# Performance work log

Measured on AMD Instinct MI355X. Metric: run time of the kernel, lower is better.

## Reference

```python
import jax, jax.numpy as jnp
import numpy as np

# Central-difference gradients on a 5D field (b, d1, d2, d3, c); slices crop
# the two non-differentiated spatial axes by 1 on each side so all outputs align.

def grad_dx(f):
    return (f[:, 2:, 1:-1, 1:-1] - f[:, :-2, 1:-1, 1:-1]) * 0.5

def grad_dy(f):
    return (f[:, 1:-1, 2:, 1:-1] - f[:, 1:-1, :-2, 1:-1]) * 0.5

def grad_dz(f):
    return (f[:, 1:-1, 1:-1, 2:] - f[:, 1:-1, 1:-1, :-2]) * 0.5


def setup_inputs() -> dict:
    key = jax.random.key(0)
    ddf = jax.random.normal(key, (4, 160, 160, 160, 3), dtype=jnp.float32)
    return {"ddf": ddf}


def reference(ddf) -> jnp.ndarray:
    # first derivatives: (b, d-2, h-2, w-2, 3)
    dfdx = grad_dx(ddf)
    dfdy = grad_dy(ddf)
    dfdz = grad_dz(ddf)
    # second derivatives: (b, d-4, h-4, w-4, 3)
    dfdxx = grad_dx(dfdx)
    dfdyy = grad_dy(dfdy)
    dfdzz = grad_dz(dfdz)
    dfdxy = grad_dy(dfdx)
    dfdyz = grad_dz(dfdy)
    dfdxz = grad_dz(dfdx)
    energy = (dfdxx ** 2 + dfdyy ** 2 + dfdzz ** 2
              + 2.0 * dfdxy ** 2 + 2.0 * dfdxz ** 2 + 2.0 * dfdyz ** 2)
    return jnp.mean(energy, axis=(1, 2, 3, 4))  # shape (batch,)
```

## Files before the change

kernel.cpp:

```cpp
#include <hip/hip_runtime.h>


typedef float F4 __attribute__((ext_vector_type(4)));

#define DIM 160
#define SX (DIM * DIM * 3)
#define SY (DIM * 3)
#define FSZ ((long long)DIM * SX)
#define TOT (4LL * FSZ)

#define ROWS 20
#define ROWU 37
#define USED_U (ROWS * ROWU)
#define SLICE_U 744
#define SLICE_F (SLICE_U * 4)
#define SLOTS 6
#define STEPS 26
#define NSEG 6
#define NMS 4
#define NYT 10
#define NBLK (4 * NSEG * NMS * NYT)
#define CPX (NBLK / 8)

__global__ __launch_bounds__(256, 2) void be_kernel(const float* __restrict__ f,
                                                    float* __restrict__ out) {
    __shared__ float lds[SLICE_F * SLOTS];
    const int tid = threadIdx.x;

    int lid = (blockIdx.x & 7) * CPX + (blockIdx.x >> 3);
    int p2 = lid / (NMS * NYT);
    int q2 = lid % (NMS * NYT);
    int b = p2 / NSEG, xseg = p2 % NSEG;
    int ms = q2 / NYT, yt = q2 % NYT;

    const int X0 = 2 + xseg * STEPS;
    const int gy0 = 16 * yt;
    const int core = 4 + 128 * ms;
    const int Gm = core - 8;
    const long long bb = (long long)b * FSZ;
    const float* fend = f + (TOT - 4);

    const int t = tid >> 4;
    const int yy = tid & 15;
    const int m0 = core + 8 * t;
    const int y = 2 + 16 * yt + yy;

    int jlo = 6 - m0; if (jlo < 0) jlo = 0;
    int jhi = 474 - m0; if (jhi > 8) jhi = 8;
    if (y >= DIM - 2) jhi = -1;

    const int rc = (yy + 2) * ROWU + 2 * t;

    auto stage = [&](int slab) {
        int slot = slab % SLOTS;
        long long gbase = bb + (long long)slab * SX + Gm;
#pragma unroll
        for (int it = 0; it < 3; ++it) {
            int c = it * 256 + tid;
            if (c < USED_U) {
                int row = c / ROWU;
                int col = c - row * ROWU;
                const float* gp = f + (gbase + (long long)(gy0 + row) * SY + 4 * col);
                gp = gp < f ? f : gp;
                gp = gp > fend ? fend : gp;
                __builtin_amdgcn_global_load_lds(
                    (const __attribute__((address_space(1))) unsigned int*)gp,
                    (__attribute__((address_space(3))) unsigned int*)
                        ((__attribute__((address_space(3))) float*)lds
                         + slot * SLICE_F + 4 * c),
                    16, 0, 0);
            }
        }
    };

    for (int d = -2; d <= 2; ++d) stage(X0 + d);
    __syncthreads();

    float e = 0.0f;
    for (int s = 0; s < STEPS; ++s) {
        int x = X0 + s;
        stage(x + 3);

        const float* L0  = lds + ((x    ) % SLOTS) * SLICE_F + 4 * rc;
        const float* Lp1 = lds + ((x + 1) % SLOTS) * SLICE_F + 4 * rc;
        const float* Lm1 = lds + ((x + 5) % SLOTS) * SLICE_F + 4 * rc;
        const float* Lp2 = lds + ((x + 2) % SLOTS) * SLICE_F + 4 * rc;
        const float* Lm2 = lds + ((x + 4) % SLOTS) * SLICE_F + 4 * rc;

        float C[24], XP[16], XM[16], YP[16], YM[16];
        F4 X2P[2], X2M[2], Y2P[2], Y2M[2], DPP[2], DPM[2], DMP[2], DMM[2];
#pragma unroll
        for (int i = 0; i < 6; ++i)
            *reinterpret_cast<F4*>(&C[4 * i]) =
                *reinterpret_cast<const F4*>(L0 + 4 * i);
#pragma unroll
        for (int i = 0; i < 4; ++i) {
            *reinterpret_cast<F4*>(&XP[4 * i]) =
                *reinterpret_cast<const F4*>(Lp1 + 4 + 4 * i);
            *reinterpret_cast<F4*>(&XM[4 * i]) =
                *reinterpret_cast<const F4*>(Lm1 + 4 + 4 * i);
            *reinterpret_cast<F4*>(&YP[4 * i]) =
                *reinterpret_cast<const F4*>(L0 + 4 * ROWU + 4 + 4 * i);
            *reinterpret_cast<F4*>(&YM[4 * i]) =
                *reinterpret_cast<const F4*>(L0 - 4 * ROWU + 4 + 4 * i);
        }
#pragma unroll
        for (int i = 0; i < 2; ++i) {
            X2P[i] = *reinterpret_cast<const F4*>(Lp2 + 8 + 4 * i);
            X2M[i] = *reinterpret_cast<const F4*>(Lm2 + 8 + 4 * i);
            Y2P[i] = *reinterpret_cast<const F4*>(L0 + 8 * ROWU + 8 + 4 * i);
            Y2M[i] = *reinterpret_cast<const F4*>(L0 - 8 * ROWU + 8 + 4 * i);
            DPP[i] = *reinterpret_cast<const F4*>(Lp1 + 4 * ROWU + 8 + 4 * i);
            DPM[i] = *reinterpret_cast<const F4*>(Lp1 - 4 * ROWU + 8 + 4 * i);
            DMP[i] = *reinterpret_cast<const F4*>(Lm1 + 4 * ROWU + 8 + 4 * i);
            DMM[i] = *reinterpret_cast<const F4*>(Lm1 - 4 * ROWU + 8 + 4 * i);
        }

#pragma unroll
        for (int j = 0; j < 8; ++j) {
            float ctr2 = 2.0f * C[j + 8];
            float dxx = (X2P[j >> 2][j & 3] + X2M[j >> 2][j & 3]) - ctr2;
            float dyy = (Y2P[j >> 2][j & 3] + Y2M[j >> 2][j & 3]) - ctr2;
            float dzz = (C[j + 14] + C[j + 2]) - ctr2;
            float dxy = (DPP[j >> 2][j & 3] - DMP[j >> 2][j & 3])
                      - (DPM[j >> 2][j & 3] - DMM[j >> 2][j & 3]);
            float dxz = (XP[j + 7] - XM[j + 7]) - (XP[j + 1] - XM[j + 1]);
            float dyz = (YP[j + 7] - YM[j + 7]) - (YP[j + 1] - YM[j + 1]);
            float dd = dxx * dxx + dyy * dyy + dzz * dzz;
            float dc = dxy * dxy + dxz * dxz + dyz * dyz;
            float msk = (j >= jlo && j < jhi) ? 1.0f : 0.0f;
            e += msk * (dd + 2.0f * dc);
        }

        __syncthreads();
    }

#pragma unroll
    for (int off = 32; off > 0; off >>= 1) e += __shfl_down(e, off, 64);

    __shared__ float ws[4];
    int lane = tid & 63;
    int wid = tid >> 6;
    if (lane == 0) ws[wid] = e;
    __syncthreads();
    if (tid == 0) {
        const float inv_count = 0.0625f / (156.0f * 156.0f * 156.0f * 3.0f);
        atomicAdd(&out[b], (ws[0] + ws[1] + ws[2] + ws[3]) * inv_count);
    }
}

extern "C" void kernel_launch(void* const* d_in, const int* in_sizes, int n_in,
                              void* d_out, int out_size, void* d_ws, size_t ws_size,
                              hipStream_t stream) {
    const float* f = (const float*)d_in[0];
    float* out = (float*)d_out;

    hipMemsetAsync(d_out, 0, out_size * sizeof(float), stream);

    be_kernel<<<dim3(NBLK), dim3(256), 0, stream>>>(f, out);
}
```

Before: 98.67 us.

## Carry x-neighbour slab values in registers across steps and precompute staging offsets

Values loaded from slab x+1 are kept in registers and reused two steps later as the x-1 operands, using two alternating register sets over a loop unrolled by two. This removes 8 of the 28 vector LDS reads per step. Per-thread global staging offsets are precomputed once, which removes the per-stage divide and modulo. The thread-to-row mapping is permuted, likely to change LDS bank access patterns. The trade-off is higher register pressure from the carried values, which could limit occupancy at two blocks per CU.

```diff
diff --git a/kernel.cpp b/kernel.cpp
--- a/kernel.cpp
+++ b/kernel.cpp
@@ -38,10 +38,11 @@
     const int core = 4 + 128 * ms;
     const int Gm = core - 8;
     const long long bb = (long long)b * FSZ;
+    const float* fbase = f + bb;
     const float* fend = f + (TOT - 4);
 
     const int t = tid >> 4;
-    const int yy = tid & 15;
+    const int yy = ((tid >> 3) & 1) | ((tid & 7) << 1);
     const int m0 = core + 8 * t;
     const int y = 2 + 16 * yt + yy;
 
@@ -51,23 +52,29 @@
 
     const int rc = (yy + 2) * ROWU + 2 * t;
 
+    long long choff[3];
+#pragma unroll
+    for (int it = 0; it < 3; ++it) {
+        int c = it * 256 + tid;
+        int row = c / ROWU, col = c - row * ROWU;
+        choff[it] = (long long)(gy0 + row) * SY + Gm + 4 * col;
+    }
+    const bool ch2ok = (512 + tid) < USED_U;
+
     auto stage = [&](int slab) {
         int slot = slab % SLOTS;
-        long long gbase = bb + (long long)slab * SX + Gm;
+        long long sb = (long long)slab * SX;
 #pragma unroll
         for (int it = 0; it < 3; ++it) {
-            int c = it * 256 + tid;
-            if (c < USED_U) {
-                int row = c / ROWU;
-                int col = c - row * ROWU;
-                const float* gp = f + (gbase + (long long)(gy0 + row) * SY + 4 * col);
+            if (it < 2 || ch2ok) {
+                const float* gp = fbase + (sb + choff[it]);
                 gp = gp < f ? f : gp;
                 gp = gp > fend ? fend : gp;
                 __builtin_amdgcn_global_load_lds(
                     (const __attribute__((address_space(1))) unsigned int*)gp,
                     (__attribute__((address_space(3))) unsigned int*)
                         ((__attribute__((address_space(3))) float*)lds
-                         + slot * SLICE_F + 4 * c),
+                         + slot * SLICE_F + 4 * (it * 256 + tid)),
                     16, 0, 0);
             }
         }
@@ -76,44 +83,53 @@
     for (int d = -2; d <= 2; ++d) stage(X0 + d);
     __syncthreads();
 
+    F4 fa_xm[4], fa_pp[2], fa_pm[2], fb_xm[4], fb_pp[2], fb_pm[2];
+    {
+        const float* Sm1 = lds + ((X0 + 5) % SLOTS) * SLICE_F + 4 * rc;
+        const float* S0  = lds + ((X0) % SLOTS) * SLICE_F + 4 * rc;
+#pragma unroll
+        for (int i = 0; i < 4; ++i) {
+            fa_xm[i] = *(const F4*)(Sm1 + 4 + 4 * i);
+            fb_xm[i] = *(const F4*)(S0 + 4 + 4 * i);
+        }
+#pragma unroll
+        for (int i = 0; i < 2; ++i) {
+            fa_pp[i] = *(const F4*)(Sm1 + 4 * ROWU + 8 + 4 * i);
+            fa_pm[i] = *(const F4*)(Sm1 - 4 * ROWU + 8 + 4 * i);
+            fb_pp[i] = *(const F4*)(S0 + 4 * ROWU + 8 + 4 * i);
+            fb_pm[i] = *(const F4*)(S0 - 4 * ROWU + 8 + 4 * i);
+        }
+    }
+
     float e = 0.0f;
-    for (int s = 0; s < STEPS; ++s) {
-        int x = X0 + s;
+
+    auto step = [&](int x, F4* Fxm, F4* Fpp, F4* Fpm) {
         stage(x + 3);
 
-        const float* L0  = lds + ((x    ) % SLOTS) * SLICE_F + 4 * rc;
+        const float* L0  = lds + ((x) % SLOTS) * SLICE_F + 4 * rc;
         const float* Lp1 = lds + ((x + 1) % SLOTS) * SLICE_F + 4 * rc;
-        const float* Lm1 = lds + ((x + 5) % SLOTS) * SLICE_F + 4 * rc;
         const float* Lp2 = lds + ((x + 2) % SLOTS) * SLICE_F + 4 * rc;
         const float* Lm2 = lds + ((x + 4) % SLOTS) * SLICE_F + 4 * rc;
 
-        float C[24], XP[16], XM[16], YP[16], YM[16];
-        F4 X2P[2], X2M[2], Y2P[2], Y2M[2], DPP[2], DPM[2], DMP[2], DMM[2];
+        float C[24], XP[16], YP[16], YM[16];
+        F4 X2P[2], X2M[2], Y2P[2], Y2M[2], PPn[2], PMn[2];
 #pragma unroll
         for (int i = 0; i < 6; ++i)
-            *reinterpret_cast<F4*>(&C[4 * i]) =
-                *reinterpret_cast<const F4*>(L0 + 4 * i);
+            *(F4*)(&C[4 * i]) = *(const F4*)(L0 + 4 * i);
 #pragma unroll
         for (int i = 0; i < 4; ++i) {
-            *reinterpret_cast<F4*>(&XP[4 * i]) =
-                *reinterpret_cast<const F4*>(Lp1 + 4 + 4 * i);
-            *reinterpret_cast<F4*>(&XM[4 * i]) =
-                *reinterpret_cast<const F4*>(Lm1 + 4 + 4 * i);
-            *reinterpret_cast<F4*>(&YP[4 * i]) =
-                *reinterpret_cast<const F4*>(L0 + 4 * ROWU + 4 + 4 * i);
-            *reinterpret_cast<F4*>(&YM[4 * i]) =
-                *reinterpret_cast<const F4*>(L0 - 4 * ROWU + 4 + 4 * i);
+            *(F4*)(&XP[4 * i]) = *(const F4*)(Lp1 + 4 + 4 * i);
+            *(F4*)(&YP[4 * i]) = *(const F4*)(L0 + 4 * ROWU + 4 + 4 * i);
+            *(F4*)(&YM[4 * i]) = *(const F4*)(L0 - 4 * ROWU + 4 + 4 * i);
         }
 #pragma unroll
         for (int i = 0; i < 2; ++i) {
-            X2P[i] = *reinterpret_cast<const F4*>(Lp2 + 8 + 4 * i);
-            X2M[i] = *reinterpret_cast<const F4*>(Lm2 + 8 + 4 * i);
-            Y2P[i] = *reinterpret_cast<const F4*>(L0 + 8 * ROWU + 8 + 4 * i);
-            Y2M[i] = *reinterpret_cast<const F4*>(L0 - 8 * ROWU + 8 + 4 * i);
-            DPP[i] = *reinterpret_cast<const F4*>(Lp1 + 4 * ROWU + 8 + 4 * i);
-            DPM[i] = *reinterpret_cast<const F4*>(Lp1 - 4 * ROWU + 8 + 4 * i);
-            DMP[i] = *reinterpret_cast<const F4*>(Lm1 + 4 * ROWU + 8 + 4 * i);
-            DMM[i] = *reinterpret_cast<const F4*>(Lm1 - 4 * ROWU + 8 + 4 * i);
+            X2P[i] = *(const F4*)(Lp2 + 8 + 4 * i);
+            X2M[i] = *(const F4*)(Lm2 + 8 + 4 * i);
+            Y2P[i] = *(const F4*)(L0 + 8 * ROWU + 8 + 4 * i);
+            Y2M[i] = *(const F4*)(L0 - 8 * ROWU + 8 + 4 * i);
+            PPn[i] = *(const F4*)(Lp1 + 4 * ROWU + 8 + 4 * i);
+            PMn[i] = *(const F4*)(Lp1 - 4 * ROWU + 8 + 4 * i);
         }
 
 #pragma unroll
@@ -122,9 +138,10 @@
             float dxx = (X2P[j >> 2][j & 3] + X2M[j >> 2][j & 3]) - ctr2;
             float dyy = (Y2P[j >> 2][j & 3] + Y2M[j >> 2][j & 3]) - ctr2;
             float dzz = (C[j + 14] + C[j + 2]) - ctr2;
-            float dxy = (DPP[j >> 2][j & 3] - DMP[j >> 2][j & 3])
-                      - (DPM[j >> 2][j & 3] - DMM[j >> 2][j & 3]);
-            float dxz = (XP[j + 7] - XM[j + 7]) - (XP[j + 1] - XM[j + 1]);
+            float dxy = (PPn[j >> 2][j & 3] - Fpp[j >> 2][j & 3])
+                      - (PMn[j >> 2][j & 3] - Fpm[j >> 2][j & 3]);
+            float dxz = (XP[j + 7] - Fxm[(j + 7) >> 2][(j + 7) & 3])
+                      - (XP[j + 1] - Fxm[(j + 1) >> 2][(j + 1) & 3]);
             float dyz = (YP[j + 7] - YM[j + 7]) - (YP[j + 1] - YM[j + 1]);
             float dd = dxx * dxx + dyy * dyy + dzz * dzz;
             float dc = dxy * dxy + dxz * dxz + dyz * dyz;
@@ -132,7 +149,17 @@
             e += msk * (dd + 2.0f * dc);
         }
 
+#pragma unroll
+        for (int i = 0; i < 4; ++i) Fxm[i] = *(F4*)(&XP[4 * i]);
+#pragma unroll
+        for (int i = 0; i < 2; ++i) { Fpp[i] = PPn[i]; Fpm[i] = PMn[i]; }
+
         __syncthreads();
+    };
+
+    for (int sp = 0; sp < STEPS / 2; ++sp) {
+        step(X0 + 2 * sp,     fa_xm, fa_pp, fa_pm);
+        step(X0 + 2 * sp + 1, fb_xm, fb_pp, fb_pm);
     }
 
 #pragma unroll
```

New measurement: 86.96 us. 11.9% less time.
